# Kernel tuning notes

Hardware: AMD Instinct MI355X
Metric: run time of the kernel (lower is better)

## Reference

```python
import jax, jax.numpy as jnp
import numpy as np

F = 16  # ConvLSTM2D filters

def hard_sigmoid(x):
    # Keras (TF2) hard_sigmoid: clip(0.2*x + 0.5, 0, 1) -- ConvLSTM2D default recurrent_activation
    return jnp.clip(0.2 * x + 0.5, 0.0, 1.0)

def convlstm_1x1(x, W, U, b, reverse):
    # x: [B,T,H,W,C]; W: [C,4F]; U: [F,4F]; b: [4F]
    # 1x1 ConvLSTM2D == per-pixel LSTM; gate order in Keras kernel: i, f, c, o
    B, T, H, Wd, C = x.shape
    xs = jnp.moveaxis(x, 1, 0)  # [T,B,H,W,C]
    h0 = jnp.zeros((B, H, Wd, F), x.dtype)
    c0 = jnp.zeros((B, H, Wd, F), x.dtype)
    def step(carry, xt):
        h, c = carry
        z = jnp.einsum('bhwc,cf->bhwf', xt, W) + jnp.einsum('bhwc,cf->bhwf', h, U) + b
        i, f, g, o = jnp.split(z, 4, axis=-1)
        i = hard_sigmoid(i); f = hard_sigmoid(f); o = hard_sigmoid(o)
        c_new = f * c + i * jnp.tanh(g)
        h_new = o * jnp.tanh(c_new)
        return (h_new, c_new), h_new
    # reverse=True: scan runs backward in time, ys aligned to input order,
    # which matches Keras Bidirectional(go_backwards + output re-reversal).
    _, hs = jax.lax.scan(step, (h0, c0), xs, reverse=reverse)
    return jnp.moveaxis(hs, 0, 1)  # [B,T,H,W,F]

def setup_inputs() -> dict:
    key = jax.random.key(0)
    ks = jax.random.split(key, 13)
    B, T, H, Wd, C = 16, 64, 32, 32, 32
    s = 0.1
    inp = {
        'inputs': jax.random.normal(ks[0], (B, T, H, Wd, C), jnp.float32),
        'Wf': jax.random.normal(ks[1], (C, 4 * F), jnp.float32) * s,
        'Uf': jax.random.normal(ks[2], (F, 4 * F), jnp.float32) * s,
        'bf': jnp.zeros((4 * F,), jnp.float32),
        'Wb': jax.random.normal(ks[3], (C, 4 * F), jnp.float32) * s,
        'Ub': jax.random.normal(ks[4], (F, 4 * F), jnp.float32) * s,
        'bb': jnp.zeros((4 * F,), jnp.float32),
        'w1': jax.random.normal(ks[5], (2 * F, 16), jnp.float32) * s,
        'b1': jnp.zeros((16,), jnp.float32),
        'w2': jax.random.normal(ks[6], (16, 16), jnp.float32) * s,
        'b2': jnp.zeros((16,), jnp.float32),
        'w3': jax.random.normal(ks[7], (16, 10), jnp.float32) * s,
        'b3': jnp.zeros((10,), jnp.float32),
    }
    return inp

def reference(inputs, Wf, Uf, bf, Wb, Ub, bb, w1, b1, w2, b2, w3, b3):
    h_fwd = convlstm_1x1(inputs, Wf, Uf, bf, reverse=False)
    h_bwd = convlstm_1x1(inputs, Wb, Ub, bb, reverse=True)
    x = jnp.concatenate([h_fwd, h_bwd], axis=-1)  # [B,T,H,W,2F]
    x = jnp.einsum('...c,cd->...d', x, w1) + b1
    x = jnp.einsum('...c,cd->...d', x, w2) + b2
    x = jnp.einsum('...c,cd->...d', x, w3) + b3
    return x  # [B,T,H,W,10]
```

## Files before the change

### kernel.cpp

```cpp
#include <hip/hip_runtime.h>
#include <hip/hip_bf16.h>
#include <cstdint>
#include <cstddef>

#define TT 64
#define CC 32
#define FF 16
#define HWSZ 1024
#define NPIX 16384

typedef __attribute__((ext_vector_type(8))) short  short8;
typedef __attribute__((ext_vector_type(4))) short  short4v;
typedef __attribute__((ext_vector_type(4))) float  f32x4;

__device__ __forceinline__ float bf2f(unsigned int u16) {
  union { unsigned int u; float f; } c;
  c.u = u16 << 16;
  return c.f;
}
__device__ __forceinline__ unsigned int f2bf(float f) {
  union { float f; unsigned int u; } c;
  c.f = f;
  unsigned int u = c.u;
  return (u + 0x7fffu + ((u >> 16) & 1u)) >> 16;
}
__device__ __forceinline__ unsigned int pkbf(float a, float b) {
  float2 f2; f2.x = a; f2.y = b;
  __hip_bfloat162 h = __float22bfloat162_rn(f2);
  union { __hip_bfloat162 h; unsigned int u; } c; c.h = h;
  return c.u;
}
__device__ __forceinline__ float clamp01(float x) {
  return fminf(fmaxf(x, 0.0f), 1.0f);
}

__device__ __forceinline__ int2 opaque_copy2(int a, int b) {
  int2 r;
  asm("v_mov_b32 %0, %2\n\tv_mov_b32 %1, %3"
      : "=&v"(r.x), "=&v"(r.y)
      : "v"(a), "v"(b));
  return r;
}

#define L2E2 2.8853900817779268f
__device__ __forceinline__ float tanh_e2(float e2arg) {
  const float e = __builtin_exp2f(e2arg);
  const float t = __builtin_amdgcn_rcpf(e + 1.0f);
  return fmaf(-2.0f, t, 1.0f);
}

__global__ __launch_bounds__(512) void fold_kernel(
    const float* __restrict__ w1, const float* __restrict__ b1,
    const float* __restrict__ w2, const float* __restrict__ b2,
    const float* __restrict__ w3, const float* __restrict__ b3,
    float* __restrict__ Wc, float* __restrict__ bc)
{
  __shared__ float w23[16 * 10];
  __shared__ float bb2[16];
  const int t = threadIdx.x;

  if (t < 160) {
    const int k = t / 10, j = t % 10;
    float s = 0.0f;
    #pragma unroll
    for (int m = 0; m < 16; ++m) s = fmaf(w2[k * 16 + m], w3[m * 10 + j], s);
    w23[t] = s;
  }
  if (t < 16) {
    float s = b2[t];
    #pragma unroll
    for (int m = 0; m < 16; ++m) s = fmaf(b1[m], w2[m * 16 + t], s);
    bb2[t] = s;
  }
  __syncthreads();
  if (t < 320) {
    const int k = t / 10, j = t % 10;
    float s = 0.0f;
    #pragma unroll
    for (int m = 0; m < 16; ++m) s = fmaf(w1[k * 16 + m], w23[m * 10 + j], s);
    Wc[t] = s;
  }
  if (t < 10) {
    float s = b3[t];
    #pragma unroll
    for (int m = 0; m < 16; ++m) s = fmaf(bb2[m], w3[m * 10 + t], s);
    bc[t] = s;
  }
}

__global__ __launch_bounds__(256, 2) void lstm_kernel(
    const float* __restrict__ x,
    const float* __restrict__ Wf, const float* __restrict__ Uf, const float* __restrict__ bfp,
    const float* __restrict__ Wb, const float* __restrict__ Ub, const float* __restrict__ bbp,
    unsigned short* __restrict__ hf_out, unsigned short* __restrict__ hb_out)
{
  const int dir = blockIdx.y;
  const float* __restrict__ Wp = dir ? Wb : Wf;
  const float* __restrict__ Up = dir ? Ub : Uf;
  const float* __restrict__ bp = dir ? bbp : bfp;
  unsigned short* __restrict__ hout = dir ? hb_out : hf_out;

  const int tid  = threadIdx.x;
  const int lane = tid & 63;
  const int wid  = tid >> 6;
  const int quad = lane >> 4;
  const int l15  = lane & 15;

  const int px  = (blockIdx.x * 4 + wid) * 16 + l15;
  const int b   = px >> 10;
  const int hwi = px & 1023;

  short8  AW[4];
  short4v AU[4];
  #pragma unroll
  for (int nt = 0; nt < 4; ++nt) {
    short8 vw;
    #pragma unroll
    for (int j = 0; j < 8; ++j) {
      const int k   = quad * 8 + j;
      const int col = nt * 16 + l15;
      vw[j] = (short)f2bf(Wp[k * 64 + col]);
    }
    AW[nt] = vw;
    short4v vu;
    #pragma unroll
    for (int j = 0; j < 4; ++j) {
      const int k   = quad * 4 + j;
      const int col = nt * 16 + l15;
      vu[j] = (short)f2bf(Up[k * 64 + col]);
    }
    AU[nt] = vu;
  }

  float bi[4], bfv[4], bgl[4], bo[4];
  #pragma unroll
  for (int r = 0; r < 4; ++r) {
    const int f = quad * 4 + r;
    bi[r]  = fmaf(bp[ 0 + f], 0.2f, 0.5f);
    bfv[r] = fmaf(bp[16 + f], 0.2f, 0.5f);
    bgl[r] = bp[32 + f] * L2E2;
    bo[r]  = fmaf(bp[48 + f], 0.2f, 0.5f);
  }

  float cst[4] = {0.f, 0.f, 0.f, 0.f};
  union BU  { short8  s8; int i[4]; };
  union BH  { short4v s4; int i[2]; };
  BH Bh; Bh.i[0] = 0; Bh.i[1] = 0;

  const int t0 = dir ? (TT - 1) : 0;
  const unsigned int pos0 = (unsigned int)((b * TT + t0) * HWSZ + hwi);
  const int xstep = dir ? -(HWSZ * CC * 4) : (HWSZ * CC * 4);
  const int hstep = dir ? -(HWSZ * 32) : (HWSZ * 32);
  unsigned int hob = pos0 * 32 + quad * 8;

  const char* xb = (const char*)x;
  char* hbb = (char*)hout;

  const unsigned int xo0 = pos0 * (CC * 4) + quad * 32;
  float4 t0a = *reinterpret_cast<const float4*>(xb + xo0);
  float4 t0b = *reinterpret_cast<const float4*>(xb + xo0 + 16);
  unsigned int xoff = xo0 + xstep;
  float4 b1a = *reinterpret_cast<const float4*>(xb + xoff);
  float4 b1b = *reinterpret_cast<const float4*>(xb + xoff + 16);
  xoff += xstep;
  float4 b2a = *reinterpret_cast<const float4*>(xb + xoff);
  float4 b2b = *reinterpret_cast<const float4*>(xb + xoff + 16);
  xoff += xstep;
  float4 b3a = *reinterpret_cast<const float4*>(xb + xoff);
  float4 b3b = *reinterpret_cast<const float4*>(xb + xoff + 16);
  xoff += xstep;
  float4 b0a = *reinterpret_cast<const float4*>(xb + xoff);
  float4 b0b = *reinterpret_cast<const float4*>(xb + xoff + 16);

  f32x4 zx[4];
  {
    BU ax;
    ax.i[0] = pkbf(t0a.x, t0a.y); ax.i[1] = pkbf(t0a.z, t0a.w);
    ax.i[2] = pkbf(t0b.x, t0b.y); ax.i[3] = pkbf(t0b.z, t0b.w);
    const f32x4 zz = {0.f, 0.f, 0.f, 0.f};
    #pragma unroll
    for (int nt = 0; nt < 4; ++nt)
      zx[nt] = __builtin_amdgcn_mfma_f32_16x16x32_bf16(AW[nt], ax.s8, zz, 0, 0, 0);
  }

  int2 sA = make_int2(0, 0), sB = make_int2(0, 0);
  int2 sC = make_int2(0, 0), sD = make_int2(0, 0);

#define STEP(S, BA, BB, SA) do {                                               \
            \
    f32x4 z_[4];                                                               \
    _Pragma("unroll")                                                          \
    for (int nt = 0; nt < 4; ++nt)                                             \
      z_[nt] = __builtin_amdgcn_mfma_f32_16x16x16bf16_1k(AU[nt], Bh.s4, zx[nt], 0, 0, 0); \
                     \
    {                                                                          \
      BU ax;                                                                   \
      ax.i[0] = pkbf(BA.x, BA.y); ax.i[1] = pkbf(BA.z, BA.w);                  \
      ax.i[2] = pkbf(BB.x, BB.y); ax.i[3] = pkbf(BB.z, BB.w);                  \
      const f32x4 zzv = {0.f, 0.f, 0.f, 0.f};                                  \
      _Pragma("unroll")                                                        \
      for (int nt = 0; nt < 4; ++nt)                                           \
        zx[nt] = __builtin_amdgcn_mfma_f32_16x16x32_bf16(AW[nt], ax.s8, zzv, 0, 0, 0); \
    }                                                                          \
          \
    if ((S) + 5 < TT) xoff += xstep;                                           \
    BA = *reinterpret_cast<const float4*>(xb + xoff);                          \
    BB = *reinterpret_cast<const float4*>(xb + xoff + 16);                     \
                              \
    float hv[4];                                                               \
    _Pragma("unroll")                                                          \
    for (int r = 0; r < 4; ++r) {                                              \
      const float ig = clamp01(fmaf(z_[0][r], 0.2f, bi[r]));                   \
      const float fg = clamp01(fmaf(z_[1][r], 0.2f, bfv[r]));                  \
      const float og = clamp01(fmaf(z_[3][r], 0.2f, bo[r]));                   \
      const float gg = tanh_e2(fmaf(z_[2][r], L2E2, bgl[r]));                  \
      cst[r] = fmaf(fg, cst[r], ig * gg);                                      \
      hv[r]  = og * tanh_e2(cst[r] * L2E2);                                    \
    }                                                                          \
            \
    Bh.i[0] = (int)pkbf(hv[0], hv[1]);                       \
    Bh.i[1] = (int)pkbf(hv[2], hv[3]);                     \
        \
    SA = opaque_copy2(Bh.i[0], Bh.i[1]);                                       \
    *reinterpret_cast<int2*>(hbb + hob) = SA;                                  \
    hob += hstep;                                                              \
  } while (0)

  for (int sb = 0; sb < TT; sb += 4) {
    STEP(sb + 0, b1a, b1b, sA);
    STEP(sb + 1, b2a, b2b, sB);
    STEP(sb + 2, b3a, b3b, sC);
    STEP(sb + 3, b0a, b0b, sD);
  }
#undef STEP
}

__global__ __launch_bounds__(256) void dense_kernel(
    const unsigned short* __restrict__ hf, const unsigned short* __restrict__ hb,
    const float* __restrict__ Wc, const float* __restrict__ bc,
    float* __restrict__ out)
{
  const int tid  = threadIdx.x;
  const int lane = tid & 63;
  const int quad = lane >> 4;
  const int l15  = lane & 15;

  short8 Bhi, Blo;
  #pragma unroll
  for (int j = 0; j < 8; ++j) {
    const int k = quad * 8 + j;
    const float v  = (l15 < 10) ? Wc[k * 10 + l15] : 0.0f;
    const unsigned int hi = f2bf(v);
    const float lo = v - bf2f(hi);
    Bhi[j] = (short)hi;
    Blo[j] = (short)f2bf(lo);
  }
  const float bcv = (l15 < 10) ? bc[l15] : 0.0f;

  const unsigned short* __restrict__ src = (quad & 2) ? hb : hf;
  const unsigned int lsub = (quad & 1) * 8;

  const unsigned int gw = (blockIdx.x * 256 + tid) >> 6;

  #pragma unroll
  for (int i = 0; i < 8; ++i) {
    const unsigned int tile  = gw * 8 + i;
    const unsigned int pos16 = tile * 16 + l15;
    const short8 A = *reinterpret_cast<const short8*>(src + pos16 * 16 + lsub);

    f32x4 acc = {bcv, bcv, bcv, bcv};
    acc = __builtin_amdgcn_mfma_f32_16x16x32_bf16(A, Bhi, acc, 0, 0, 0);
    acc = __builtin_amdgcn_mfma_f32_16x16x32_bf16(A, Blo, acc, 0, 0, 0);

    if (l15 < 10) {
      const unsigned int rowbase = tile * 16 + quad * 4;
      #pragma unroll
      for (int r = 0; r < 4; ++r) {
        out[(size_t)(rowbase + r) * 10 + l15] = acc[r];
      }
    }
  }
}

extern "C" void kernel_launch(void* const* d_in, const int* in_sizes, int n_in,
                              void* d_out, int out_size, void* d_ws, size_t ws_size,
                              hipStream_t stream) {
  const float* x   = (const float*)d_in[0];
  const float* Wf  = (const float*)d_in[1];
  const float* Uf  = (const float*)d_in[2];
  const float* bfp = (const float*)d_in[3];
  const float* Wb  = (const float*)d_in[4];
  const float* Ub  = (const float*)d_in[5];
  const float* bbp = (const float*)d_in[6];
  const float* w1  = (const float*)d_in[7];
  const float* b1  = (const float*)d_in[8];
  const float* w2  = (const float*)d_in[9];
  const float* b2  = (const float*)d_in[10];
  const float* w3  = (const float*)d_in[11];
  const float* b3  = (const float*)d_in[12];

  unsigned short* hfbuf = (unsigned short*)d_ws;
  unsigned short* hbbuf = hfbuf + (size_t)NPIX * TT * FF;
  float* Wc = (float*)(hbbuf + (size_t)NPIX * TT * FF);
  float* bc = Wc + 320;

  fold_kernel<<<1, 512, 0, stream>>>(w1, b1, w2, b2, w3, b3, Wc, bc);

  lstm_kernel<<<dim3(256, 2), 256, 0, stream>>>(x, Wf, Uf, bfp, Wb, Ub, bbp, hfbuf, hbbuf);

  dense_kernel<<<2048, 256, 0, stream>>>(hfbuf, hbbuf, Wc, bc, (float*)d_out);
}
```

Baseline: 273.6 us.

## Prefetch x in 8-step chunks and fold dense weights inside dense kernel

The LSTM recurrence now loads x for eight timesteps at once, eight steps ahead, and packs them to bf16 in bulk, replacing the per-step prefetch ring four deep. This aims to hide global load latency behind more of the recurrent chain, at the cost of more live registers. The separate fold kernel is removed. Every dense block now recomputes the folded 32x10 weights and bias into shared memory, which saves one launch but adds redundant per-block work and barriers.

```diff
diff --git a/kernel.cpp b/kernel.cpp
--- a/kernel.cpp
+++ b/kernel.cpp
@@ -32,6 +32,13 @@
 }
 __device__ __forceinline__ float clamp01(float x) {
   return fminf(fmaxf(x, 0.0f), 1.0f);
+}
+
+#define L2E2 2.8853900817779268f
+__device__ __forceinline__ float tanh_e2(float e2arg) {
+  const float e = __builtin_exp2f(e2arg);
+  const float t = __builtin_amdgcn_rcpf(e + 1.0f);
+  return fmaf(-2.0f, t, 1.0f);
 }
 
 __device__ __forceinline__ int2 opaque_copy2(int a, int b) {
@@ -40,52 +47,6 @@
       : "=&v"(r.x), "=&v"(r.y)
       : "v"(a), "v"(b));
   return r;
-}
-
-#define L2E2 2.8853900817779268f
-__device__ __forceinline__ float tanh_e2(float e2arg) {
-  const float e = __builtin_exp2f(e2arg);
-  const float t = __builtin_amdgcn_rcpf(e + 1.0f);
-  return fmaf(-2.0f, t, 1.0f);
-}
-
-__global__ __launch_bounds__(512) void fold_kernel(
-    const float* __restrict__ w1, const float* __restrict__ b1,
-    const float* __restrict__ w2, const float* __restrict__ b2,
-    const float* __restrict__ w3, const float* __restrict__ b3,
-    float* __restrict__ Wc, float* __restrict__ bc)
-{
-  __shared__ float w23[16 * 10];
-  __shared__ float bb2[16];
-  const int t = threadIdx.x;
-
-  if (t < 160) {
-    const int k = t / 10, j = t % 10;
-    float s = 0.0f;
-    #pragma unroll
-    for (int m = 0; m < 16; ++m) s = fmaf(w2[k * 16 + m], w3[m * 10 + j], s);
-    w23[t] = s;
-  }
-  if (t < 16) {
-    float s = b2[t];
-    #pragma unroll
-    for (int m = 0; m < 16; ++m) s = fmaf(b1[m], w2[m * 16 + t], s);
-    bb2[t] = s;
-  }
-  __syncthreads();
-  if (t < 320) {
-    const int k = t / 10, j = t % 10;
-    float s = 0.0f;
-    #pragma unroll
-    for (int m = 0; m < 16; ++m) s = fmaf(w1[k * 16 + m], w23[m * 10 + j], s);
-    Wc[t] = s;
-  }
-  if (t < 10) {
-    float s = b3[t];
-    #pragma unroll
-    for (int m = 0; m < 16; ++m) s = fmaf(bb2[m], w3[m * 10 + t], s);
-    bc[t] = s;
-  }
 }
 
 __global__ __launch_bounds__(256, 2) void lstm_kernel(
@@ -153,59 +114,51 @@
   const int hstep = dir ? -(HWSZ * 32) : (HWSZ * 32);
   unsigned int hob = pos0 * 32 + quad * 8;
 
-  const char* xb = (const char*)x;
-  char* hbb = (char*)hout;
+  const char* xb  = (const char*)x;
+  char*       hbb = (char*)hout;
 
   const unsigned int xo0 = pos0 * (CC * 4) + quad * 32;
-  float4 t0a = *reinterpret_cast<const float4*>(xb + xo0);
-  float4 t0b = *reinterpret_cast<const float4*>(xb + xo0 + 16);
-  unsigned int xoff = xo0 + xstep;
-  float4 b1a = *reinterpret_cast<const float4*>(xb + xoff);
-  float4 b1b = *reinterpret_cast<const float4*>(xb + xoff + 16);
-  xoff += xstep;
-  float4 b2a = *reinterpret_cast<const float4*>(xb + xoff);
-  float4 b2b = *reinterpret_cast<const float4*>(xb + xoff + 16);
-  xoff += xstep;
-  float4 b3a = *reinterpret_cast<const float4*>(xb + xoff);
-  float4 b3b = *reinterpret_cast<const float4*>(xb + xoff + 16);
-  xoff += xstep;
-  float4 b0a = *reinterpret_cast<const float4*>(xb + xoff);
-  float4 b0b = *reinterpret_cast<const float4*>(xb + xoff + 16);
+  unsigned int xoff = xo0;
+
+  f32x4 F0a, F0b, F1a, F1b, F2a, F2b, F3a, F3b;
+  f32x4 F4a, F4b, F5a, F5b, F6a, F6b, F7a, F7b;
+  BU P0, P1, P2, P3, P4, P5, P6, P7;
+
+#define LOADPAIR(FA, FB) do {                                                  \
+    FA = *reinterpret_cast<const f32x4*>(xb + xoff);                           \
+    FB = *reinterpret_cast<const f32x4*>(xb + xoff + 16);                      \
+    xoff += xstep;                                                             \
+  } while (0)
+#define LOADCHUNK() do {                                                       \
+    LOADPAIR(F0a, F0b); LOADPAIR(F1a, F1b); LOADPAIR(F2a, F2b);                \
+    LOADPAIR(F3a, F3b); LOADPAIR(F4a, F4b); LOADPAIR(F5a, F5b);                \
+    LOADPAIR(F6a, F6b); LOADPAIR(F7a, F7b);                                    \
+  } while (0)
+#define PACKONE(P, FA, FB) do {                                                \
+    P.i[0] = pkbf(FA[0], FA[1]); P.i[1] = pkbf(FA[2], FA[3]);                  \
+    P.i[2] = pkbf(FB[0], FB[1]); P.i[3] = pkbf(FB[2], FB[3]);                  \
+  } while (0)
+
+  LOADCHUNK();
 
   f32x4 zx[4];
-  {
-    BU ax;
-    ax.i[0] = pkbf(t0a.x, t0a.y); ax.i[1] = pkbf(t0a.z, t0a.w);
-    ax.i[2] = pkbf(t0b.x, t0b.y); ax.i[3] = pkbf(t0b.z, t0b.w);
-    const f32x4 zz = {0.f, 0.f, 0.f, 0.f};
-    #pragma unroll
-    for (int nt = 0; nt < 4; ++nt)
-      zx[nt] = __builtin_amdgcn_mfma_f32_16x16x32_bf16(AW[nt], ax.s8, zz, 0, 0, 0);
-  }
-
-  int2 sA = make_int2(0, 0), sB = make_int2(0, 0);
-  int2 sC = make_int2(0, 0), sD = make_int2(0, 0);
-
-#define STEP(S, BA, BB, SA) do {                                               \
-            \
+
+  int2 g0 = {0,0}, g1 = {0,0}, g2 = {0,0}, g3 = {0,0};
+  int2 g4 = {0,0}, g5 = {0,0}, g6 = {0,0}, g7 = {0,0};
+
+#define STEP(PN, GS) do {                                                      \
+                              \
     f32x4 z_[4];                                                               \
     _Pragma("unroll")                                                          \
     for (int nt = 0; nt < 4; ++nt)                                             \
       z_[nt] = __builtin_amdgcn_mfma_f32_16x16x16bf16_1k(AU[nt], Bh.s4, zx[nt], 0, 0, 0); \
-                     \
+                                           \
     {                                                                          \
-      BU ax;                                                                   \
-      ax.i[0] = pkbf(BA.x, BA.y); ax.i[1] = pkbf(BA.z, BA.w);                  \
-      ax.i[2] = pkbf(BB.x, BB.y); ax.i[3] = pkbf(BB.z, BB.w);                  \
       const f32x4 zzv = {0.f, 0.f, 0.f, 0.f};                                  \
       _Pragma("unroll")                                                        \
       for (int nt = 0; nt < 4; ++nt)                                           \
-        zx[nt] = __builtin_amdgcn_mfma_f32_16x16x32_bf16(AW[nt], ax.s8, zzv, 0, 0, 0); \
+        zx[nt] = __builtin_amdgcn_mfma_f32_16x16x32_bf16(AW[nt], PN.s8, zzv, 0, 0, 0); \
     }                                                                          \
-          \
-    if ((S) + 5 < TT) xoff += xstep;                                           \
-    BA = *reinterpret_cast<const float4*>(xb + xoff);                          \
-    BB = *reinterpret_cast<const float4*>(xb + xoff + 16);                     \
                               \
     float hv[4];                                                               \
     _Pragma("unroll")                                                          \
@@ -217,30 +170,103 @@
       cst[r] = fmaf(fg, cst[r], ig * gg);                                      \
       hv[r]  = og * tanh_e2(cst[r] * L2E2);                                    \
     }                                                                          \
-            \
-    Bh.i[0] = (int)pkbf(hv[0], hv[1]);                       \
-    Bh.i[1] = (int)pkbf(hv[2], hv[3]);                     \
-        \
-    SA = opaque_copy2(Bh.i[0], Bh.i[1]);                                       \
-    *reinterpret_cast<int2*>(hbb + hob) = SA;                                  \
+                                     \
+    Bh.i[0] = (int)pkbf(hv[0], hv[1]);                                         \
+    Bh.i[1] = (int)pkbf(hv[2], hv[3]);                                         \
+                             \
+    GS = opaque_copy2(Bh.i[0], Bh.i[1]);                                       \
+    *reinterpret_cast<int2*>(hbb + hob) = GS;                                  \
     hob += hstep;                                                              \
   } while (0)
 
-  for (int sb = 0; sb < TT; sb += 4) {
-    STEP(sb + 0, b1a, b1b, sA);
-    STEP(sb + 1, b2a, b2b, sB);
-    STEP(sb + 2, b3a, b3b, sC);
-    STEP(sb + 3, b0a, b0b, sD);
+#define STEPLAST(GS) do {                                                      \
+    f32x4 z_[4];                                                               \
+    _Pragma("unroll")                                                          \
+    for (int nt = 0; nt < 4; ++nt)                                             \
+      z_[nt] = __builtin_amdgcn_mfma_f32_16x16x16bf16_1k(AU[nt], Bh.s4, zx[nt], 0, 0, 0); \
+    float hv[4];                                                               \
+    _Pragma("unroll")                                                          \
+    for (int r = 0; r < 4; ++r) {                                              \
+      const float ig = clamp01(fmaf(z_[0][r], 0.2f, bi[r]));                   \
+      const float fg = clamp01(fmaf(z_[1][r], 0.2f, bfv[r]));                  \
+      const float og = clamp01(fmaf(z_[3][r], 0.2f, bo[r]));                   \
+      const float gg = tanh_e2(fmaf(z_[2][r], L2E2, bgl[r]));                  \
+      cst[r] = fmaf(fg, cst[r], ig * gg);                                      \
+      hv[r]  = og * tanh_e2(cst[r] * L2E2);                                    \
+    }                                                                          \
+    Bh.i[0] = (int)pkbf(hv[0], hv[1]);                                         \
+    Bh.i[1] = (int)pkbf(hv[2], hv[3]);                                         \
+    GS = opaque_copy2(Bh.i[0], Bh.i[1]);                                       \
+    *reinterpret_cast<int2*>(hbb + hob) = GS;                                  \
+    hob += hstep;                                                              \
+  } while (0)
+
+  #pragma clang loop unroll(disable)
+  for (int ch = 0; ch < 8; ++ch) {
+    PACKONE(P0, F0a, F0b); PACKONE(P1, F1a, F1b);
+    PACKONE(P2, F2a, F2b); PACKONE(P3, F3a, F3b);
+    PACKONE(P4, F4a, F4b); PACKONE(P5, F5a, F5b);
+    PACKONE(P6, F6a, F6b); PACKONE(P7, F7a, F7b);
+    if (ch < 7) { LOADCHUNK(); }
+    {
+      const f32x4 zzv = {0.f, 0.f, 0.f, 0.f};
+      #pragma unroll
+      for (int nt = 0; nt < 4; ++nt)
+        zx[nt] = __builtin_amdgcn_mfma_f32_16x16x32_bf16(AW[nt], P0.s8, zzv, 0, 0, 0);
+    }
+    STEP(P1, g0); STEP(P2, g1); STEP(P3, g2); STEP(P4, g3);
+    STEP(P5, g4); STEP(P6, g5); STEP(P7, g6); STEPLAST(g7);
   }
 #undef STEP
+#undef STEPLAST
+#undef LOADPAIR
+#undef LOADCHUNK
+#undef PACKONE
 }
 
 __global__ __launch_bounds__(256) void dense_kernel(
     const unsigned short* __restrict__ hf, const unsigned short* __restrict__ hb,
-    const float* __restrict__ Wc, const float* __restrict__ bc,
+    const float* __restrict__ w1, const float* __restrict__ b1,
+    const float* __restrict__ w2, const float* __restrict__ b2,
+    const float* __restrict__ w3, const float* __restrict__ b3,
     float* __restrict__ out)
 {
+  __shared__ float Wc[320];
+  __shared__ float bcs[10];
+  __shared__ float w23[160];
+  __shared__ float bb2[16];
+
   const int tid  = threadIdx.x;
+
+  for (int i = tid; i < 160; i += 256) {
+    const int k = i / 10, j = i % 10;
+    float s = 0.0f;
+    #pragma unroll
+    for (int m = 0; m < 16; ++m) s = fmaf(w2[k * 16 + m], w3[m * 10 + j], s);
+    w23[i] = s;
+  }
+  if (tid < 16) {
+    float s = b2[tid];
+    #pragma unroll
+    for (int m = 0; m < 16; ++m) s = fmaf(b1[m], w2[m * 16 + tid], s);
+    bb2[tid] = s;
+  }
+  __syncthreads();
+  for (int i = tid; i < 320; i += 256) {
+    const int k = i / 10, j = i % 10;
+    float s = 0.0f;
+    #pragma unroll
+    for (int m = 0; m < 16; ++m) s = fmaf(w1[k * 16 + m], w23[m * 10 + j], s);
+    Wc[i] = s;
+  }
+  if (tid < 10) {
+    float s = b3[tid];
+    #pragma unroll
+    for (int m = 0; m < 16; ++m) s = fmaf(bb2[m], w3[m * 10 + tid], s);
+    bcs[tid] = s;
+  }
+  __syncthreads();
+
   const int lane = tid & 63;
   const int quad = lane >> 4;
   const int l15  = lane & 15;
@@ -255,7 +281,7 @@
     Bhi[j] = (short)hi;
     Blo[j] = (short)f2bf(lo);
   }
-  const float bcv = (l15 < 10) ? bc[l15] : 0.0f;
+  const float bcv = (l15 < 10) ? bcs[l15] : 0.0f;
 
   const unsigned short* __restrict__ src = (quad & 2) ? hb : hf;
   const unsigned int lsub = (quad & 1) * 8;
@@ -301,12 +327,10 @@
 
   unsigned short* hfbuf = (unsigned short*)d_ws;
   unsigned short* hbbuf = hfbuf + (size_t)NPIX * TT * FF;
-  float* Wc = (float*)(hbbuf + (size_t)NPIX * TT * FF);
-  float* bc = Wc + 320;
-
-  fold_kernel<<<1, 512, 0, stream>>>(w1, b1, w2, b2, w3, b3, Wc, bc);
-
-  lstm_kernel<<<dim3(256, 2), 256, 0, stream>>>(x, Wf, Uf, bfp, Wb, Ub, bbp, hfbuf, hbbuf);
-
-  dense_kernel<<<2048, 256, 0, stream>>>(hfbuf, hbbuf, Wc, bc, (float*)d_out);
-}
+
+  lstm_kernel<<<dim3(256, 2), 256, 0, stream>>>(x, Wf, Uf, bfp, Wb, Ub, bbp,
+                                                hfbuf, hbbuf);
+
+  dense_kernel<<<2048, 256, 0, stream>>>(hfbuf, hbbuf,
+                                         w1, b1, w2, b2, w3, b3, (float*)d_out);
+}
```

New measurement: 278.8 us. No clear change (+1.9%).

## Fold dense weights inside dense kernel and stagger LSTM wave start times

Applied to the files above, without the earlier changes.

Removes the separate single-block fold_kernel launch. Each dense_kernel block now recomputes the folded w1·w2·w3 weights and bias into shared memory. Separately, LSTM waves sleep for a staggered number of cycles at start, which aims to desynchronise memory and compute phases across waves. The costs are redundant fold work in every dense block, two extra barriers per block, and deliberate idle time at the start of the LSTM kernel.

```diff
diff --git a/kernel.cpp b/kernel.cpp
--- a/kernel.cpp
+++ b/kernel.cpp
@@ -47,45 +47,6 @@
   const float e = __builtin_exp2f(e2arg);
   const float t = __builtin_amdgcn_rcpf(e + 1.0f);
   return fmaf(-2.0f, t, 1.0f);
-}
-
-__global__ __launch_bounds__(512) void fold_kernel(
-    const float* __restrict__ w1, const float* __restrict__ b1,
-    const float* __restrict__ w2, const float* __restrict__ b2,
-    const float* __restrict__ w3, const float* __restrict__ b3,
-    float* __restrict__ Wc, float* __restrict__ bc)
-{
-  __shared__ float w23[16 * 10];
-  __shared__ float bb2[16];
-  const int t = threadIdx.x;
-
-  if (t < 160) {
-    const int k = t / 10, j = t % 10;
-    float s = 0.0f;
-    #pragma unroll
-    for (int m = 0; m < 16; ++m) s = fmaf(w2[k * 16 + m], w3[m * 10 + j], s);
-    w23[t] = s;
-  }
-  if (t < 16) {
-    float s = b2[t];
-    #pragma unroll
-    for (int m = 0; m < 16; ++m) s = fmaf(b1[m], w2[m * 16 + t], s);
-    bb2[t] = s;
-  }
-  __syncthreads();
-  if (t < 320) {
-    const int k = t / 10, j = t % 10;
-    float s = 0.0f;
-    #pragma unroll
-    for (int m = 0; m < 16; ++m) s = fmaf(w1[k * 16 + m], w23[m * 10 + j], s);
-    Wc[t] = s;
-  }
-  if (t < 10) {
-    float s = b3[t];
-    #pragma unroll
-    for (int m = 0; m < 16; ++m) s = fmaf(bb2[m], w3[m * 10 + t], s);
-    bc[t] = s;
-  }
 }
 
 __global__ __launch_bounds__(256, 2) void lstm_kernel(
@@ -105,6 +66,11 @@
   const int wid  = tid >> 6;
   const int quad = lane >> 4;
   const int l15  = lane & 15;
+
+  {
+    const int sid = (int)((blockIdx.x + (unsigned)wid) & 7u);
+    for (int i = 0; i < sid; ++i) __builtin_amdgcn_s_sleep(15);
+  }
 
   const int px  = (blockIdx.x * 4 + wid) * 16 + l15;
   const int b   = px >> 10;
@@ -237,10 +203,47 @@
 
 __global__ __launch_bounds__(256) void dense_kernel(
     const unsigned short* __restrict__ hf, const unsigned short* __restrict__ hb,
-    const float* __restrict__ Wc, const float* __restrict__ bc,
+    const float* __restrict__ w1, const float* __restrict__ b1,
+    const float* __restrict__ w2, const float* __restrict__ b2,
+    const float* __restrict__ w3, const float* __restrict__ b3,
     float* __restrict__ out)
 {
+  __shared__ float Wc[320];
+  __shared__ float bcs[10];
+  __shared__ float w23[160];
+  __shared__ float bb2[16];
+
   const int tid  = threadIdx.x;
+
+  for (int i = tid; i < 160; i += 256) {
+    const int k = i / 10, j = i % 10;
+    float s = 0.0f;
+    #pragma unroll
+    for (int m = 0; m < 16; ++m) s = fmaf(w2[k * 16 + m], w3[m * 10 + j], s);
+    w23[i] = s;
+  }
+  if (tid < 16) {
+    float s = b2[tid];
+    #pragma unroll
+    for (int m = 0; m < 16; ++m) s = fmaf(b1[m], w2[m * 16 + tid], s);
+    bb2[tid] = s;
+  }
+  __syncthreads();
+  for (int i = tid; i < 320; i += 256) {
+    const int k = i / 10, j = i % 10;
+    float s = 0.0f;
+    #pragma unroll
+    for (int m = 0; m < 16; ++m) s = fmaf(w1[k * 16 + m], w23[m * 10 + j], s);
+    Wc[i] = s;
+  }
+  if (tid < 10) {
+    float s = b3[tid];
+    #pragma unroll
+    for (int m = 0; m < 16; ++m) s = fmaf(bb2[m], w3[m * 10 + tid], s);
+    bcs[tid] = s;
+  }
+  __syncthreads();
+
   const int lane = tid & 63;
   const int quad = lane >> 4;
   const int l15  = lane & 15;
@@ -255,7 +258,7 @@
     Bhi[j] = (short)hi;
     Blo[j] = (short)f2bf(lo);
   }
-  const float bcv = (l15 < 10) ? bc[l15] : 0.0f;
+  const float bcv = (l15 < 10) ? bcs[l15] : 0.0f;
 
   const unsigned short* __restrict__ src = (quad & 2) ? hb : hf;
   const unsigned int lsub = (quad & 1) * 8;
@@ -301,12 +304,10 @@
 
   unsigned short* hfbuf = (unsigned short*)d_ws;
   unsigned short* hbbuf = hfbuf + (size_t)NPIX * TT * FF;
-  float* Wc = (float*)(hbbuf + (size_t)NPIX * TT * FF);
-  float* bc = Wc + 320;
-
-  fold_kernel<<<1, 512, 0, stream>>>(w1, b1, w2, b2, w3, b3, Wc, bc);
-
-  lstm_kernel<<<dim3(256, 2), 256, 0, stream>>>(x, Wf, Uf, bfp, Wb, Ub, bbp, hfbuf, hbbuf);
-
-  dense_kernel<<<2048, 256, 0, stream>>>(hfbuf, hbbuf, Wc, bc, (float*)d_out);
-}
+
+  lstm_kernel<<<dim3(256, 2), 256, 0, stream>>>(x, Wf, Uf, bfp, Wb, Ub, bbp,
+                                                hfbuf, hbbuf);
+
+  dense_kernel<<<2048, 256, 0, stream>>>(hfbuf, hbbuf,
+                                         w1, b1, w2, b2, w3, b3, (float*)d_out);
+}
```

Result: no change. 274.5 us (+0.4%).
